# Kernel tuning notes

Measured on AMD Instinct MI355X. Metric: run time of the kernel, lower is better.

Reference implementation:

```python
import jax, jax.numpy as jnp
import numpy as np

EPS = 1e-5
COMMITMENT_WEIGHT = 1.0


def setup_inputs() -> dict:
    key = jax.random.key(0)
    k1, k2 = jax.random.split(key)
    x = jax.random.normal(k1, (4, 4096, 128), dtype=jnp.float32)
    codebook = jax.random.normal(k2, (8192, 128), dtype=jnp.float32)
    return {"x": x, "codebook": codebook}


def _layernorm(x):
    # LayerNorm over last dim, elementwise_affine=False, eps=1e-5
    mu = jnp.mean(x, axis=-1, keepdims=True)
    var = jnp.mean(jnp.square(x - mu), axis=-1, keepdims=True)
    return (x - mu) * jax.lax.rsqrt(var + EPS)


def reference(x, codebook):
    b, n, d = x.shape
    xn = _layernorm(x)                      # [b, n, d]
    flat = xn.reshape(b * n, d)             # [bn, d]
    x2 = jnp.sum(flat * flat, axis=-1, keepdims=True)          # [bn, 1]
    e2 = jnp.sum(codebook * codebook, axis=-1)                  # [K]
    dots = jnp.einsum('nd,kd->nk', flat, codebook)              # [bn, K]
    distances = x2 - 2.0 * dots + e2[None, :]                   # [bn, K]
    embed_ind = jnp.argmin(distances, axis=-1)                  # [bn]
    quantize = codebook[embed_ind].reshape(b, n, d)             # gather
    embed_ind = embed_ind.reshape(b, n)
    loss = jnp.mean(jnp.square(quantize - xn)) * COMMITMENT_WEIGHT
    # straight-through
    quantize_st = xn + jax.lax.stop_gradient(quantize - xn)
    return (quantize_st, embed_ind, loss)
```

## Files before the change

kernel.cpp:

```cpp
#include <hip/hip_runtime.h>
#include <hip/hip_fp16.h>
#include <math.h>

typedef _Float16 half8  __attribute__((ext_vector_type(8)));
typedef _Float16 half2v __attribute__((ext_vector_type(2)));
typedef float   floatx4 __attribute__((ext_vector_type(4)));

#define ROWS   16384
#define DIM    128
#define KCODES 8192
#define NSPLIT 16
#define KSPLIT (KCODES / NSPLIT)
#define NGROUP (KSPLIT / 16)
#define MTILE  256
#define THR    0.3f

__device__ __forceinline__ void async_copy16(const void* src, void* dst_lds) {
  __builtin_amdgcn_global_load_lds((const __attribute__((address_space(1))) void*)src,
                                   (__attribute__((address_space(3))) void*)dst_lds,
                                   16, 0, 0);
}

__global__ __launch_bounds__(256) void prep_kernel(
    const float* __restrict__ cb, const float* __restrict__ x,
    _Float16* __restrict__ ehg, float* __restrict__ e2g,
    _Float16* __restrict__ xnh, float* __restrict__ out_loss)
{
  int tid = threadIdx.x;
  int L = tid & 63;
  int bx = blockIdx.x;
  if (bx == 0 && tid == 0) *out_loss = 0.f;
  if (bx < KCODES / 4) {
    int row = bx * 4 + (tid >> 6);
    float2 v = ((const float2*)(cb + (size_t)row * DIM))[L];
    float s2 = v.x * v.x + v.y * v.y;
    #pragma unroll
    for (int m = 1; m < 64; m <<= 1) s2 += __shfl_xor(s2, m);
    if (L == 0) e2g[row] = -0.5f * s2;
    half2v hi = {(_Float16)v.x, (_Float16)v.y};
    ((half2v*)(ehg + (size_t)row * DIM))[L] = hi;
  } else {
    int row = (bx - KCODES / 4) * 4 + (tid >> 6);
    float2 xv = ((const float2*)(x + (size_t)row * DIM))[L];
    float s = xv.x + xv.y;
    #pragma unroll
    for (int m = 1; m < 64; m <<= 1) s += __shfl_xor(s, m);
    float mu = s * (1.0f / 128.0f);
    float dx = xv.x - mu, dy = xv.y - mu;
    float s2 = dx * dx + dy * dy;
    #pragma unroll
    for (int m = 1; m < 64; m <<= 1) s2 += __shfl_xor(s2, m);
    float rstd = 1.0f / sqrtf(s2 * (1.0f / 128.0f) + 1e-5f);
    half2v hv = {(_Float16)(dx * rstd), (_Float16)(dy * rstd)};
    ((half2v*)(xnh + (size_t)row * DIM))[L] = hv;
  }
}

__global__ __launch_bounds__(256, 2) void argmin_kernel(
    const _Float16* __restrict__ xnh, const _Float16* __restrict__ ehg,
    const float* __restrict__ e2g,
    float* __restrict__ b1p, int* __restrict__ i1p,
    float* __restrict__ b2p, int* __restrict__ i2p)
{
  __shared__ _Float16 ebuf[4][2][16][128];
  __shared__ float e2l[KSPLIT];

  int tid = threadIdx.x;
  int w = tid >> 6, L = tid & 63, c = L & 15, q = L >> 4;
  int bx = blockIdx.x;
  int mt = bx & (ROWS / MTILE - 1);
  int ns = bx >> 6;
  int rowbase = mt * MTILE + w * 64;
  int code0 = ns * KSPLIT;

  half8 ah[4][4];
  #pragma unroll
  for (int g = 0; g < 4; ++g) {
    const _Float16* xr = xnh + (size_t)(rowbase + g * 16 + c) * DIM;
    #pragma unroll
    for (int ks = 0; ks < 4; ++ks)
      ah[g][ks] = *(const half8*)(xr + ks * 32 + q * 8);
  }

  if (tid < KSPLIT / 4) {
    float4 v = ((const float4*)(e2g + code0))[tid];
    float4 o = {256.f + v.x, 256.f + v.y, 256.f + v.z, 256.f + v.w};
    ((float4*)e2l)[tid] = o;
  }

  const _Float16* gsrc[4];
  _Float16*       ldst[2][4];
  #pragma unroll
  for (int it = 0; it < 4; ++it) {
    int cid = it * 64 + L;
    int n   = cid >> 4;
    int kcs = cid & 15;
    int kc  = kcs ^ (n & 7);
    gsrc[it]    = ehg + (size_t)(code0 + n) * DIM + kc * 8;
    ldst[0][it] = &ebuf[w][0][0][0] + cid * 8;
    ldst[1][it] = &ebuf[w][1][0][0] + cid * 8;
  }
  __syncthreads();

  auto stage = [&](int g, int ring) {
    #pragma unroll
    for (int it = 0; it < 4; ++it)
      async_copy16(gsrc[it] + (size_t)g * 16 * DIM, ldst[ring][it]);
  };
  stage(0, 0); stage(1, 1);

  unsigned k1[4][4], k2[4][4];
  #pragma unroll
  for (int g = 0; g < 4; ++g)
    #pragma unroll
    for (int r = 0; r < 4; ++r) { k1[g][r] = 0u; k2[g][r] = 0u; }

  for (int g = 0; g < NGROUP; ++g) {
    if (g + 1 < NGROUP) asm volatile("s_waitcnt vmcnt(4)" ::: "memory");
    else                asm volatile("s_waitcnt vmcnt(0)" ::: "memory");

    const _Float16* buf = &ebuf[w][g & 1][0][0];
    float e2v = e2l[(size_t)g * 16 + c];
    half8 bh[4];
    #pragma unroll
    for (int ks = 0; ks < 4; ++ks)
      bh[ks] = *(const half8*)(buf + (size_t)c * 128 + ((ks * 4 + q) ^ (c & 7)) * 8);

    unsigned gp = (unsigned)g;
    #pragma unroll
    for (int gg = 0; gg < 4; ++gg) {
      floatx4 acc = {e2v, e2v, e2v, e2v};
      #pragma unroll
      for (int ks = 0; ks < 4; ++ks)
        acc = __builtin_amdgcn_mfma_f32_16x16x32_f16(ah[gg][ks], bh[ks], acc, 0, 0, 0);
      #pragma unroll
      for (int r = 0; r < 4; ++r) {
        unsigned kk = (__float_as_uint(acc[r]) & 0xFFFFFFC0u) | gp;
        unsigned tt = kk < k1[gg][r] ? kk : k1[gg][r];
        k1[gg][r] = kk > k1[gg][r] ? kk : k1[gg][r];
        k2[gg][r] = tt > k2[gg][r] ? tt : k2[gg][r];
      }
    }
    if (g + 2 < NGROUP) {
      asm volatile("s_waitcnt lgkmcnt(0)" ::: "memory");
      stage(g + 2, g & 1);
    }
  }

  #pragma unroll
  for (int gg = 0; gg < 4; ++gg)
    #pragma unroll
    for (int r = 0; r < 4; ++r) {
      float s1 = __uint_as_float(k1[gg][r] & 0xFFFFFFC0u) - 256.f;
      float s2 = __uint_as_float(k2[gg][r] & 0xFFFFFFC0u) - 256.f;
      int   j1 = code0 + (int)(k1[gg][r] & 63u) * 16 + c;
      int   j2 = code0 + (int)(k2[gg][r] & 63u) * 16 + c;
      #pragma unroll
      for (int m = 1; m < 16; m <<= 1) {
        float o1 = __shfl_xor(s1, m); int oj1 = __shfl_xor(j1, m);
        float o2 = __shfl_xor(s2, m); int oj2 = __shfl_xor(j2, m);
        if (o1 > s1) {
          bool t = (s1 >= o2);
          s2 = t ? s1 : o2;  j2 = t ? j1 : oj2;
          s1 = o1; j1 = oj1;
        } else {
          bool t = (o1 >= s2);
          s2 = t ? o1 : s2;  j2 = t ? oj1 : j2;
        }
      }
      if (c == 0) {
        int row = rowbase + gg * 16 + q * 4 + r;
        b1p[(size_t)row * NSPLIT + ns] = s1; i1p[(size_t)row * NSPLIT + ns] = j1;
        b2p[(size_t)row * NSPLIT + ns] = s2; i2p[(size_t)row * NSPLIT + ns] = j2;
      }
    }
}

__global__ __launch_bounds__(256) void gather_loss_kernel(
    const float* __restrict__ x, const float* __restrict__ cb,
    const float* __restrict__ e2g,
    const float* __restrict__ b1p, const int* __restrict__ i1p,
    const float* __restrict__ b2p, const int* __restrict__ i2p,
    float* __restrict__ out_q, float* __restrict__ out_ind,
    float* __restrict__ out_loss)
{
  __shared__ float lsum[4];
  int tid = threadIdx.x;
  int L = tid & 63;
  int w = tid >> 6;
  int row = blockIdx.x * 4 + w;

  int k  = L & 31;
  int qd = L >> 5;

  int ci = 0; float cv = -3.4e38f;
  if (L < 16)      { ci = i1p[(size_t)row * NSPLIT + L];        cv = b1p[(size_t)row * NSPLIT + L]; }
  else if (L < 32) { ci = i2p[(size_t)row * NSPLIT + (L - 16)]; cv = b2p[(size_t)row * NSPLIT + (L - 16)]; }
  int   idxk = __shfl(ci, k);
  float tvk  = __shfl(cv, k);

  float tmax = tvk;
  #pragma unroll
  for (int m = 1; m < 32; m <<= 1) tmax = fmaxf(tmax, __shfl_xor(tmax, m));
  bool keep = tvk >= tmax - THR;
  unsigned long long mb = __ballot(keep);

  float2 xv = ((const float2*)(x + (size_t)row * DIM))[L];
  float s = xv.x + xv.y;
  #pragma unroll
  for (int m = 1; m < 64; m <<= 1) s += __shfl_xor(s, m);
  float mu = s * (1.0f / 128.0f);
  float dx = xv.x - mu, dy = xv.y - mu;
  float s2 = dx * dx + dy * dy;
  #pragma unroll
  for (int m = 1; m < 64; m <<= 1) s2 += __shfl_xor(s2, m);
  float rstd = 1.0f / sqrtf(s2 * (1.0f / 128.0f) + 1e-5f);

  int bi;
  if (__popcll(mb) == 2) {
    int lsel = (int)__ffsll(mb) - 1;
    bi = __shfl(idxk, lsel);
  } else {
    float p = 0.f;
    if (keep) {
      const float4* xr4 = (const float4*)(x  + (size_t)row  * DIM);
      const float4* er4 = (const float4*)(cb + (size_t)idxk * DIM);
      #pragma unroll
      for (int j = 0; j < 16; ++j) {
        float4 a = xr4[qd * 16 + j];
        float4 e = er4[qd * 16 + j];
        p += (a.x - mu) * e.x + (a.y - mu) * e.y + (a.z - mu) * e.z + (a.w - mu) * e.w;
      }
      p *= rstd;
    }
    p += __shfl_xor(p, 32);
    float t = keep ? p + e2g[idxk] : -3.4e38f;
    bi = idxk;
    #pragma unroll
    for (int m = 1; m < 32; m <<= 1) {
      float ot = __shfl_xor(t, m);
      int   oi = __shfl_xor(bi, m);
      if (ot > t || (ot == t && oi < bi)) { t = ot; bi = oi; }
    }
  }

  float2 qv = ((const float2*)(cb + (size_t)bi * DIM))[L];
  ((float2*)out_q)[(size_t)row * 64 + L] = qv;
  float xn0 = dx * rstd, xn1 = dy * rstd;
  float e0 = qv.x - xn0, e1 = qv.y - xn1;
  float le = e0 * e0 + e1 * e1;
  #pragma unroll
  for (int m = 1; m < 64; m <<= 1) le += __shfl_xor(le, m);
  if (L == 0) {
    lsum[w] = le;
    out_ind[row] = (float)bi;
  }
  __syncthreads();
  if (tid == 0)
    atomicAdd(out_loss, (lsum[0] + lsum[1] + lsum[2] + lsum[3]) * (1.0f / ((float)ROWS * DIM)));
}

extern "C" void kernel_launch(void* const* d_in, const int* in_sizes, int n_in,
                              void* d_out, int out_size, void* d_ws, size_t ws_size,
                              hipStream_t stream)
{
  const float* x  = (const float*)d_in[0];
  const float* cb = (const float*)d_in[1];

  char* ws = (char*)d_ws;
  _Float16* ehg = (_Float16*)(ws + 0);
  float*    e2g = (float*)   (ws + 2097152);
  float*    b1p = (float*)   (ws + 2129920);
  int*      i1p = (int*)     (ws + 3178496);
  float*    b2p = (float*)   (ws + 4227072);
  int*      i2p = (int*)     (ws + 5275648);

  float* out_q    = (float*)d_out;
  float* out_ind  = out_q + (size_t)ROWS * DIM;
  float* out_loss = out_ind + ROWS;

  _Float16* xnh = (_Float16*)out_q;

  prep_kernel<<<KCODES / 4 + ROWS / 4, 256, 0, stream>>>(cb, x, ehg, e2g, xnh, out_loss);
  argmin_kernel<<<(ROWS / MTILE) * NSPLIT, 256, 0, stream>>>(xnh, ehg, e2g, b1p, i1p, b2p, i2p);
  gather_loss_kernel<<<ROWS / 4, 256, 0, stream>>>(x, cb, e2g, b1p, i1p, b2p, i2p, out_q, out_ind, out_loss);
}
```

Measured before the change: 180.5 us.

## Load codebook fragments directly from global into registers, dropping LDS staging

Removes the per-wave LDS ring buffer filled by async global-to-LDS copies. Each lane now loads its B-operand half8 fragments straight from global memory into two register sets, double-buffered by hand across pairs of groups. This cuts LDS use, the swizzled LDS reads and the explicit waitcnt handling, which may allow more occupancy. The cost is more register pressure, and the loads now rely on L1/L2 hits because each wave re-reads codebook rows that other waves also read.

```diff
diff --git a/kernel.cpp b/kernel.cpp
--- a/kernel.cpp
+++ b/kernel.cpp
@@ -15,12 +15,6 @@
 #define MTILE  256
 #define THR    0.3f
 
-__device__ __forceinline__ void async_copy16(const void* src, void* dst_lds) {
-  __builtin_amdgcn_global_load_lds((const __attribute__((address_space(1))) void*)src,
-                                   (__attribute__((address_space(3))) void*)dst_lds,
-                                   16, 0, 0);
-}
-
 __global__ __launch_bounds__(256) void prep_kernel(
     const float* __restrict__ cb, const float* __restrict__ x,
     _Float16* __restrict__ ehg, float* __restrict__ e2g,
@@ -62,7 +56,6 @@
     float* __restrict__ b1p, int* __restrict__ i1p,
     float* __restrict__ b2p, int* __restrict__ i2p)
 {
-  __shared__ _Float16 ebuf[4][2][16][128];
   __shared__ float e2l[KSPLIT];
 
   int tid = threadIdx.x;
@@ -87,27 +80,9 @@
     float4 o = {256.f + v.x, 256.f + v.y, 256.f + v.z, 256.f + v.w};
     ((float4*)e2l)[tid] = o;
   }
-
-  const _Float16* gsrc[4];
-  _Float16*       ldst[2][4];
-  #pragma unroll
-  for (int it = 0; it < 4; ++it) {
-    int cid = it * 64 + L;
-    int n   = cid >> 4;
-    int kcs = cid & 15;
-    int kc  = kcs ^ (n & 7);
-    gsrc[it]    = ehg + (size_t)(code0 + n) * DIM + kc * 8;
-    ldst[0][it] = &ebuf[w][0][0][0] + cid * 8;
-    ldst[1][it] = &ebuf[w][1][0][0] + cid * 8;
-  }
   __syncthreads();
 
-  auto stage = [&](int g, int ring) {
-    #pragma unroll
-    for (int it = 0; it < 4; ++it)
-      async_copy16(gsrc[it] + (size_t)g * 16 * DIM, ldst[ring][it]);
-  };
-  stage(0, 0); stage(1, 1);
+  const _Float16* bsrc = ehg + (size_t)(code0 + c) * DIM + q * 8;
 
   unsigned k1[4][4], k2[4][4];
   #pragma unroll
@@ -115,37 +90,44 @@
     #pragma unroll
     for (int r = 0; r < 4; ++r) { k1[g][r] = 0u; k2[g][r] = 0u; }
 
-  for (int g = 0; g < NGROUP; ++g) {
-    if (g + 1 < NGROUP) asm volatile("s_waitcnt vmcnt(4)" ::: "memory");
-    else                asm volatile("s_waitcnt vmcnt(0)" ::: "memory");
-
-    const _Float16* buf = &ebuf[w][g & 1][0][0];
-    float e2v = e2l[(size_t)g * 16 + c];
-    half8 bh[4];
-    #pragma unroll
-    for (int ks = 0; ks < 4; ++ks)
-      bh[ks] = *(const half8*)(buf + (size_t)c * 128 + ((ks * 4 + q) ^ (c & 7)) * 8);
-
-    unsigned gp = (unsigned)g;
-    #pragma unroll
-    for (int gg = 0; gg < 4; ++gg) {
-      floatx4 acc = {e2v, e2v, e2v, e2v};
+  half8 bA[4], bB[4];
+  #pragma unroll
+  for (int ks = 0; ks < 4; ++ks) bA[ks] = *(const half8*)(bsrc + ks * 32);
+
+  #define COMPUTE(GIDX, BREG)                                                   \
+    {                                                                           \
+      float e2v = e2l[(GIDX) * 16 + c];                                         \
+      unsigned gp = (unsigned)(GIDX);                                           \
+      _Pragma("unroll")                                                         \
+      for (int gg = 0; gg < 4; ++gg) {                                          \
+        floatx4 acc = {e2v, e2v, e2v, e2v};                                     \
+        _Pragma("unroll")                                                       \
+        for (int ks = 0; ks < 4; ++ks)                                          \
+          acc = __builtin_amdgcn_mfma_f32_16x16x32_f16(ah[gg][ks], BREG[ks],    \
+                                                       acc, 0, 0, 0);           \
+        _Pragma("unroll")                                                       \
+        for (int r = 0; r < 4; ++r) {                                           \
+          unsigned kk = (__float_as_uint(acc[r]) & 0xFFFFFFC0u) | gp;           \
+          unsigned tt = kk < k1[gg][r] ? kk : k1[gg][r];                        \
+          k1[gg][r] = kk > k1[gg][r] ? kk : k1[gg][r];                          \
+          k2[gg][r] = tt > k2[gg][r] ? tt : k2[gg][r];                          \
+        }                                                                       \
+      }                                                                         \
+    }
+
+  for (int g = 0; g < NGROUP; g += 2) {
+    const _Float16* p1 = bsrc + (size_t)(g + 1) * 16 * DIM;
+    #pragma unroll
+    for (int ks = 0; ks < 4; ++ks) bB[ks] = *(const half8*)(p1 + ks * 32);
+    COMPUTE(g, bA);
+    if (g + 2 < NGROUP) {
+      const _Float16* p2 = bsrc + (size_t)(g + 2) * 16 * DIM;
       #pragma unroll
-      for (int ks = 0; ks < 4; ++ks)
-        acc = __builtin_amdgcn_mfma_f32_16x16x32_f16(ah[gg][ks], bh[ks], acc, 0, 0, 0);
-      #pragma unroll
-      for (int r = 0; r < 4; ++r) {
-        unsigned kk = (__float_as_uint(acc[r]) & 0xFFFFFFC0u) | gp;
-        unsigned tt = kk < k1[gg][r] ? kk : k1[gg][r];
-        k1[gg][r] = kk > k1[gg][r] ? kk : k1[gg][r];
-        k2[gg][r] = tt > k2[gg][r] ? tt : k2[gg][r];
-      }
-    }
-    if (g + 2 < NGROUP) {
-      asm volatile("s_waitcnt lgkmcnt(0)" ::: "memory");
-      stage(g + 2, g & 1);
-    }
-  }
+      for (int ks = 0; ks < 4; ++ks) bA[ks] = *(const half8*)(p2 + ks * 32);
+    }
+    COMPUTE(g + 1, bB);
+  }
+  #undef COMPUTE
 
   #pragma unroll
   for (int gg = 0; gg < 4; ++gg)
```

Result: slower. 202.5 us (+12.2%).
